# Kernel tuning notes

Hardware: AMD Instinct MI355X
Metric: run time of the kernel (lower is better)

The kernel has to match this reference:

```python
import jax, jax.numpy as jnp
import numpy as np

B, S, DM, DC, L, NS = 4, 2048, 2048, 512, 4, 5  # batch, seq, d_model, d_cortical, n_layers, n_settle


def _ln(x, g, b):
    # torch nn.LayerNorm, eps=1e-5
    m = x.mean(-1, keepdims=True)
    v = ((x - m) ** 2).mean(-1, keepdims=True)
    return (x - m) * jax.lax.rsqrt(v + 1e-5) * g + b


def setup_inputs() -> dict:
    key = jax.random.key(0)
    ks = jax.random.split(key, 20)
    f = lambda k, sh: jax.random.normal(k, sh, jnp.float32) * 0.02
    return dict(
        qwen_final_hidden=jax.random.normal(ks[0], (B, S, DM), jnp.float32),
        obs=jax.random.normal(ks[1], (4, B, S, DM), jnp.float32),
        proj_W=f(ks[2], (4, DC, DM)), proj_b=f(ks[3], (4, DC)),
        fuse_W=f(ks[4], (DC, 4 * DC)), fuse_b=f(ks[5], (DC,)),
        up_W=f(ks[6], (L, DC, DC)), up_b=f(ks[7], (L, DC)),
        lateral_W=f(ks[8], (L, DC, DC)), lateral_b=f(ks[9], (L, DC)),
        precision_logit=f(ks[10], (L, DC)),
        ln_g=jnp.ones((L, DC), jnp.float32), ln_b=jnp.zeros((L, DC), jnp.float32),
        down_W=f(ks[11], (L - 1, DC, DC)), down_b=f(ks[12], (L - 1, DC)),
        out1_W=f(ks[13], (DC, DC)), out1_b=f(ks[14], (DC,)),
        out2_W=f(ks[15], (DM, DC)), out2_b=f(ks[16], (DM,)),
    )


def reference(qwen_final_hidden, obs, proj_W, proj_b, fuse_W, fuse_b,
              up_W, up_b, lateral_W, lateral_b, precision_logit,
              ln_g, ln_b, down_W, down_b, out1_W, out1_b, out2_W, out2_b):
    b, s, dm = qwen_final_hidden.shape
    # per-observed-layer input projections, concatenated along features
    proj = jnp.einsum('obsd,ocd->bsoc', obs, proj_W) + proj_b  # (B,S,4,DC)
    cat = proj.reshape(b, s, -1)
    fused = cat @ fuse_W.T + fuse_b                             # (B,S,DC)
    x0 = fused.reshape(b * s, DC)                               # per-token cortical input

    prec = jax.nn.sigmoid(precision_logit)                      # (L,DC)

    # initial bottom-up pass: activations = compress(x)
    acts = []
    x = x0
    for i in range(L):
        x = _ln(x @ up_W[i].T + up_b[i], ln_g[i], ln_b[i])
        acts.append(x)

    # settling iterations
    for _ in range(NS):
        # top-down predictions computed from pre-sweep activations
        preds = [None] * L
        for i in range(L - 1, 0, -1):
            if i < L - 1:  # top layer has no top-down weights
                preds[i - 1] = acts[i] @ down_W[i].T + down_b[i]
        x = x0
        for i in range(L):
            compressed = _ln(x @ up_W[i].T + up_b[i], ln_g[i], ln_b[i])
            target = preds[i] if preds[i] is not None else acts[i]
            werr = (compressed - target) * prec[i]
            lateral = acts[i] @ lateral_W[i].T + lateral_b[i]
            acts[i] = _ln(acts[i] + 0.5 * werr + 0.1 * lateral, ln_g[i], ln_b[i])
            x = acts[i]

    top = acts[-1]
    h = jax.nn.gelu(top @ out1_W.T + out1_b, approximate=False)
    correction = (h @ out2_W.T + out2_b).reshape(b, s, dm)
    return qwen_final_hidden + correction
```

## Files before the change

kernel.cpp:

```cpp
#include <hip/hip_runtime.h>
#include <hip/hip_bf16.h>
#include <math.h>

#define NTOK 8192
#define DMD  2048
#define DCC  512
#define TOKH 4194304

typedef __attribute__((ext_vector_type(8))) short short8;
typedef __attribute__((ext_vector_type(4))) float f32x4;

__device__ inline float bf2f(unsigned short u) {
    union { unsigned int i; float f; } x; x.i = ((unsigned int)u) << 16; return x.f;
}
__device__ inline unsigned short f2bf(float f) {
    union { float f; unsigned int i; } x; x.f = f;
    unsigned int u = x.i;
    return (unsigned short)((u + 0x7fffu + ((u >> 16) & 1u)) >> 16);
}

typedef const __attribute__((address_space(1))) unsigned int* gas1_t;
typedef __attribute__((address_space(3))) unsigned int* las3_t;
__device__ inline void async16(const void* g, void* l) {
    __builtin_amdgcn_global_load_lds(
        (gas1_t)g,
        (las3_t)(unsigned int)(unsigned long long)l, 16, 0, 0);
}

__global__ __launch_bounds__(256)
void cvt_kernel(const float* __restrict__ s, unsigned short* __restrict__ d, int n4)
{
    int i = blockIdx.x * 256 + threadIdx.x;
    if (i >= n4) return;
    float4 v = ((const float4*)s)[i];
    ushort4 o;
    o.x = f2bf(v.x); o.y = f2bf(v.y); o.z = f2bf(v.z); o.w = f2bf(v.w);
    ((ushort4*)d)[i] = o;
}

struct CvtArgs { const float* src[7]; };

__global__ __launch_bounds__(256)
void wcvt_kernel(CvtArgs ca, unsigned short* __restrict__ dst)
{
    const int total = 2359296;
    for (int i = blockIdx.x * 256 + threadIdx.x; i < total; i += gridDim.x * 256) {
        const float* sp; int base;
        if      (i < 1048576) { sp = ca.src[0]; base = 0;       }
        else if (i < 1310720) { sp = ca.src[1]; base = 1048576; }
        else if (i < 1572864) { sp = ca.src[2]; base = 1310720; }
        else if (i < 1835008) { sp = ca.src[3]; base = 1572864; }
        else if (i < 2031616) { sp = ca.src[4]; base = 1835008; }
        else if (i < 2097152) { sp = ca.src[5]; base = 2031616; }
        else                  { sp = ca.src[6]; base = 2097152; }
        float4 v = ((const float4*)sp)[i - base];
        ushort4 o;
        o.x = f2bf(v.x); o.y = f2bf(v.y); o.z = f2bf(v.z); o.w = f2bf(v.w);
        ((ushort4*)dst)[i] = o;
    }
}

struct GArgs {
    const unsigned short* A[6];
    const unsigned short* W[6];
    const float*          bias[6];
    const float*          add[6];
    void*                 C[6];
};

template<bool OUTF32, bool GELU>
__global__ __launch_bounds__(256)
void gemm16(GArgs ga, int lda, int ldw, int ldadd, int ldc, int K)
{
    __shared__ unsigned short As[128 * 32];
    __shared__ unsigned short Bs[128 * 32];

    const int z    = blockIdx.z;
    const int tid  = threadIdx.x;
    const int wave = tid >> 6;
    const int lane = tid & 63;

    const int nwg   = gridDim.x * gridDim.y;
    const int bid   = blockIdx.y * gridDim.x + blockIdx.x;
    const int swz   = (bid & 7) * (nwg >> 3) + (bid >> 3);
    const int bn    = (swz % gridDim.x) * 128;
    const int bm    = (swz / gridDim.x) * 128;

    const int wr   = wave >> 1;
    const int wc   = wave & 1;

    const unsigned short* Ap = ga.A[z];
    const unsigned short* Wp = ga.W[z];

    const int lrow = lane >> 2;
    const int lcol = (lane & 3) * 8;

    f32x4 acc[4][4] = {};

    for (int k0 = 0; k0 < K; k0 += 32) {
        #pragma unroll
        for (int r = 0; r < 2; ++r) {
            int c = wave + r * 4;
            async16(Ap + (size_t)(bm + c * 16 + lrow) * lda + k0 + lcol, As + c * 512);
            async16(Wp + (size_t)(bn + c * 16 + lrow) * ldw + k0 + lcol, Bs + c * 512);
        }
        __syncthreads();

        short8 af[4], bfr[4];
        #pragma unroll
        for (int i = 0; i < 4; ++i) {
            af[i]  = *(const short8*)&As[(wr * 64 + i * 16 + (lane & 15)) * 32 + (lane >> 4) * 8];
            bfr[i] = *(const short8*)&Bs[(wc * 64 + i * 16 + (lane & 15)) * 32 + (lane >> 4) * 8];
        }
        #pragma unroll
        for (int mi = 0; mi < 4; ++mi)
            #pragma unroll
            for (int ni = 0; ni < 4; ++ni)
                acc[mi][ni] = __builtin_amdgcn_mfma_f32_16x16x32_bf16(
                    af[mi], bfr[ni], acc[mi][ni], 0, 0, 0);
        __syncthreads();
    }

    const float* bias = ga.bias[z];
    const float* add  = ga.add[z];
    #pragma unroll
    for (int ni = 0; ni < 4; ++ni) {
        int col = bn + wc * 64 + ni * 16 + (lane & 15);
        float bv = bias ? bias[col] : 0.0f;
        #pragma unroll
        for (int mi = 0; mi < 4; ++mi) {
            #pragma unroll
            for (int r = 0; r < 4; ++r) {
                int row = bm + wr * 64 + mi * 16 + (lane >> 4) * 4 + r;
                float vv = acc[mi][ni][r] + bv;
                if (GELU) vv = 0.5f * vv * (1.0f + erff(vv * 0.7071067811865475f));
                if (OUTF32) {
                    if (add) vv += add[(size_t)row * ldadd + col];
                    ((float*)ga.C[z])[(size_t)row * ldc + col] = vv;
                } else {
                    ((unsigned short*)ga.C[z])[(size_t)row * ldc + col] = f2bf(vv);
                }
            }
        }
    }
}

__device__ inline int csw(int rl, int col) {
    int s = ((rl >> 2) & 3) ^ (rl & 3);
    return rl * 512 + (col ^ (s << 4));
}

template<int MODE>
__global__ __launch_bounds__(512)
void gemm_fused(const unsigned short* __restrict__ Ap,
                const unsigned short* __restrict__ Wp,
                const float* __restrict__ bias,
                const float* __restrict__ g,
                const float* __restrict__ b,
                const unsigned short* a_in,
                const unsigned short* t_in,
                const unsigned short* __restrict__ lat_in,
                const float* __restrict__ logit,
                unsigned short* outp)
{
    __shared__ unsigned short Bs[2][512 * 32];
    __shared__ unsigned short As2[2][32 * 32];
    __shared__ float red[2][8][32];

    const int tid  = threadIdx.x;
    const int wave = tid >> 6;
    const int lane = tid & 63;
    const int lrow = lane >> 2;
    const int lc8  = (lane & 3) * 8;
    const int bm   = blockIdx.x * 32;
    const int l15  = lane & 15;
    const int lh   = lane >> 4;

    f32x4 acc[2][4] = {};

    if (wave < 2)
        async16(Ap + (size_t)(bm + wave * 16 + lrow) * DCC + lc8, &As2[0][wave * 512]);
    #pragma unroll
    for (int r = 0; r < 4; ++r)
        async16(Wp + (size_t)((r * 8 + wave) * 16 + lrow) * DCC + lc8,
                &Bs[0][(r * 8 + wave) * 512]);
    __syncthreads();

    for (int t = 0; t < 16; ++t) {
        const int cur = t & 1;
        if (t < 15) {
            const int k0 = (t + 1) * 32;
            if (wave < 2)
                async16(Ap + (size_t)(bm + wave * 16 + lrow) * DCC + k0 + lc8,
                        &As2[cur ^ 1][wave * 512]);
            #pragma unroll
            for (int r = 0; r < 4; ++r)
                async16(Wp + (size_t)((r * 8 + wave) * 16 + lrow) * DCC + k0 + lc8,
                        &Bs[cur ^ 1][(r * 8 + wave) * 512]);
        }
        short8 af[2], bfr[4];
        #pragma unroll
        for (int mi = 0; mi < 2; ++mi)
            af[mi] = *(const short8*)&As2[cur][(mi * 16 + l15) * 32 + lh * 8];
        #pragma unroll
        for (int ni = 0; ni < 4; ++ni)
            bfr[ni] = *(const short8*)&Bs[cur][(wave * 64 + ni * 16 + l15) * 32 + lh * 8];
        #pragma unroll
        for (int mi = 0; mi < 2; ++mi)
            #pragma unroll
            for (int ni = 0; ni < 4; ++ni)
                acc[mi][ni] = __builtin_amdgcn_mfma_f32_16x16x32_bf16(
                    af[mi], bfr[ni], acc[mi][ni], 0, 0, 0);
        __syncthreads();
    }

    float bv[4], gv[4], bbv[4];
    #pragma unroll
    for (int ni = 0; ni < 4; ++ni) {
        int col = wave * 64 + ni * 16 + l15;
        bv[ni] = bias[col]; gv[ni] = g[col]; bbv[ni] = b[col];
    }

    float ps[2][4], pq[2][4];
    #pragma unroll
    for (int mi = 0; mi < 2; ++mi)
        #pragma unroll
        for (int rr = 0; rr < 4; ++rr) {
            float s = 0.f, q = 0.f;
            #pragma unroll
            for (int ni = 0; ni < 4; ++ni) {
                float v = acc[mi][ni][rr] + bv[ni];
                acc[mi][ni][rr] = v;
                s += v; q += v * v;
            }
            #pragma unroll
            for (int off = 1; off < 16; off <<= 1) {
                s += __shfl_xor(s, off, 64);
                q += __shfl_xor(q, off, 64);
            }
            ps[mi][rr] = s; pq[mi][rr] = q;
        }
    if (l15 == 0) {
        #pragma unroll
        for (int mi = 0; mi < 2; ++mi)
            #pragma unroll
            for (int rr = 0; rr < 4; ++rr) {
                int rl = mi * 16 + lh * 4 + rr;
                red[0][wave][rl] = ps[mi][rr];
                red[1][wave][rl] = pq[mi][rr];
            }
    }
    __syncthreads();

    unsigned short* compS = &Bs[0][0];
    #pragma unroll
    for (int mi = 0; mi < 2; ++mi)
        #pragma unroll
        for (int rr = 0; rr < 4; ++rr) {
            int rl = mi * 16 + lh * 4 + rr;
            float s = 0.f, q = 0.f;
            #pragma unroll
            for (int w = 0; w < 8; ++w) { s += red[0][w][rl]; q += red[1][w][rl]; }
            float m1 = s * (1.0f / DCC);
            float r1 = rsqrtf(q * (1.0f / DCC) - m1 * m1 + 1e-5f);
            #pragma unroll
            for (int ni = 0; ni < 4; ++ni) {
                int col = wave * 64 + ni * 16 + l15;
                compS[csw(rl, col)] = f2bf((acc[mi][ni][rr] - m1) * r1 * gv[ni] + bbv[ni]);
            }
        }
    __syncthreads();

    const int c0 = lane * 8;
    if constexpr (MODE == 0) {
        #pragma unroll
        for (int rr = 0; rr < 4; ++rr) {
            const int rl = wave * 4 + rr;
            const size_t gbase = (size_t)(bm + rl) * DCC + c0;
            short8 cm = *(const short8*)&compS[csw(rl, c0)];
            *(short8*)(outp + gbase) = cm;
        }
    } else {
        float gr[8], br[8], pr[8];
        {
            float4 g0 = *(const float4*)(g + c0),     g1 = *(const float4*)(g + c0 + 4);
            float4 b0 = *(const float4*)(b + c0),     b1 = *(const float4*)(b + c0 + 4);
            float4 p0 = *(const float4*)(logit + c0), p1 = *(const float4*)(logit + c0 + 4);
            float gt[8] = {g0.x,g0.y,g0.z,g0.w,g1.x,g1.y,g1.z,g1.w};
            float bt[8] = {b0.x,b0.y,b0.z,b0.w,b1.x,b1.y,b1.z,b1.w};
            float pt[8] = {p0.x,p0.y,p0.z,p0.w,p1.x,p1.y,p1.z,p1.w};
            #pragma unroll
            for (int j = 0; j < 8; ++j) {
                gr[j] = gt[j]; br[j] = bt[j];
                pr[j] = 1.0f / (1.0f + __expf(-pt[j]));
            }
        }
        #pragma unroll
        for (int rr = 0; rr < 4; ++rr) {
            const int rl = wave * 4 + rr;
            const size_t gbase = (size_t)(bm + rl) * DCC + c0;
            short8 cm = *(const short8*)&compS[csw(rl, c0)];
            short8 ar = *(const short8*)(a_in + gbase);
            short8 tr = *(const short8*)(t_in + gbase);
            short8 lr = *(const short8*)(lat_in + gbase);
            float tv[8], s = 0.f, q = 0.f;
            #pragma unroll
            for (int j = 0; j < 8; ++j) {
                float val = bf2f((unsigned short)ar[j])
                          + 0.5f * (bf2f((unsigned short)cm[j]) - bf2f((unsigned short)tr[j])) * pr[j]
                          + 0.1f * bf2f((unsigned short)lr[j]);
                tv[j] = val; s += val; q += val * val;
            }
            #pragma unroll
            for (int off = 1; off < 64; off <<= 1) {
                s += __shfl_xor(s, off, 64);
                q += __shfl_xor(q, off, 64);
            }
            float m2 = s * (1.0f / DCC);
            float r2 = rsqrtf(q * (1.0f / DCC) - m2 * m2 + 1e-5f);
            short8 o;
            #pragma unroll
            for (int j = 0; j < 8; ++j)
                o[j] = (short)f2bf((tv[j] - m2) * r2 * gr[j] + br[j]);
            *(short8*)(outp + gbase) = o;
        }
    }
}

extern "C" void kernel_launch(void* const* d_in, const int* in_sizes, int n_in,
                              void* d_out, int out_size, void* d_ws, size_t ws_size,
                              hipStream_t stream)
{
    const float* qwen   = (const float*)d_in[0];
    const float* obs    = (const float*)d_in[1];
    const float* proj_W = (const float*)d_in[2];
    const float* proj_b = (const float*)d_in[3];
    const float* fuse_W = (const float*)d_in[4];
    const float* fuse_b = (const float*)d_in[5];
    const float* up_W   = (const float*)d_in[6];
    const float* up_b   = (const float*)d_in[7];
    const float* lat_W  = (const float*)d_in[8];
    const float* lat_b  = (const float*)d_in[9];
    const float* plogit = (const float*)d_in[10];
    const float* ln_g   = (const float*)d_in[11];
    const float* ln_b   = (const float*)d_in[12];
    const float* down_W = (const float*)d_in[13];
    const float* down_b = (const float*)d_in[14];
    const float* out1_W = (const float*)d_in[15];
    const float* out1_b = (const float*)d_in[16];
    const float* out2_W = (const float*)d_in[17];
    const float* out2_b = (const float*)d_in[18];
    float* out = (float*)d_out;

    unsigned short* wsu = (unsigned short*)d_ws;
    unsigned short* catbuf = wsu;
    unsigned short* x0b    = wsu + 16777216;
    unsigned short* acts16[4] = {
        wsu + 20971520, wsu + 20971520 + TOKH,
        wsu + 20971520 + 2 * TOKH, wsu + 20971520 + 3 * TOKH };
    unsigned short* w16    = wsu + 37748736;
    unsigned short* projW16 = w16;
    unsigned short* fuseW16 = w16 + 4194304;
    unsigned short* upW16   = w16 + 5242880;
    unsigned short* latW16  = w16 + 6291456;
    unsigned short* downW16 = w16 + 7340032;
    unsigned short* out1W16 = w16 + 8126464;
    unsigned short* out2W16 = w16 + 8388608;
    unsigned short* obs16   = wsu + 47185920;
    unsigned short* h16     = catbuf;

    unsigned short* outu = (unsigned short*)d_out;
    unsigned short* pred16a = outu;
    unsigned short* pred16b = outu + TOKH;
    unsigned short* lat16[4] = { outu + 2*TOKH, outu + 3*TOKH, outu + 4*TOKH, outu + 5*TOKH };

    dim3 blk(256);
    dim3 blk512(512);

    {
        CvtArgs ca;
        ca.src[0] = proj_W; ca.src[1] = fuse_W; ca.src[2] = up_W;
        ca.src[3] = lat_W;  ca.src[4] = down_W; ca.src[5] = out1_W;
        ca.src[6] = out2_W;
        wcvt_kernel<<<dim3(2048), blk, 0, stream>>>(ca, w16);
    }

    {
        int n4 = (4 * NTOK * DMD) / 4;
        cvt_kernel<<<dim3(n4 / 256), blk, 0, stream>>>(obs, obs16, n4);
        GArgs a{};
        for (int o = 0; o < 4; ++o) {
            a.A[o]    = obs16 + (size_t)o * NTOK * DMD;
            a.W[o]    = projW16 + (size_t)o * DCC * DMD;
            a.bias[o] = proj_b + o * DCC;
            a.C[o]    = catbuf + o * DCC;
        }
        gemm16<false, false><<<dim3(DCC/128, NTOK/128, 4), blk, 0, stream>>>(
            a, DMD, DMD, 0, 4 * DCC, DMD);
    }
    {
        GArgs a{};
        a.A[0] = catbuf; a.W[0] = fuseW16; a.bias[0] = fuse_b; a.C[0] = x0b;
        gemm16<false, false><<<dim3(DCC/128, NTOK/128, 1), blk, 0, stream>>>(
            a, 4 * DCC, 4 * DCC, 0, DCC, 4 * DCC);
    }

    dim3 fgrid(NTOK / 32);

    for (int i = 0; i < 4; ++i) {
        gemm_fused<0><<<fgrid, blk512, 0, stream>>>(
            (i == 0) ? x0b : acts16[i - 1],
            upW16 + (size_t)i * DCC * DCC, up_b + i * DCC,
            ln_g + i * DCC, ln_b + i * DCC,
            nullptr, nullptr, nullptr, nullptr, acts16[i]);
    }

    for (int s = 0; s < 5; ++s) {
        {
            GArgs a{};
            a.A[0] = acts16[1]; a.W[0] = downW16 + (size_t)1 * DCC * DCC;
            a.bias[0] = down_b + 1 * DCC; a.C[0] = pred16a;
            a.A[1] = acts16[2]; a.W[1] = downW16 + (size_t)2 * DCC * DCC;
            a.bias[1] = down_b + 2 * DCC; a.C[1] = pred16b;
            for (int i = 0; i < 4; ++i) {
                a.A[2 + i] = acts16[i];
                a.W[2 + i] = latW16 + (size_t)i * DCC * DCC;
                a.bias[2 + i] = lat_b + i * DCC;
                a.C[2 + i] = lat16[i];
            }
            gemm16<false, false><<<dim3(DCC/128, NTOK/128, 6), blk, 0, stream>>>(
                a, DCC, DCC, 0, DCC, DCC);
        }
        for (int i = 0; i < 4; ++i) {
            const unsigned short* tgt =
                (i == 0) ? pred16a : (i == 1) ? pred16b : acts16[i];
            gemm_fused<1><<<fgrid, blk512, 0, stream>>>(
                (i == 0) ? x0b : acts16[i - 1],
                upW16 + (size_t)i * DCC * DCC, up_b + i * DCC,
                ln_g + i * DCC, ln_b + i * DCC,
                acts16[i], tgt, lat16[i], plogit + i * DCC, acts16[i]);
        }
    }

    {
        GArgs a{};
        a.A[0] = acts16[3]; a.W[0] = out1W16; a.bias[0] = out1_b; a.C[0] = h16;
        gemm16<false, true><<<dim3(DCC/128, NTOK/128, 1), blk, 0, stream>>>(
            a, DCC, DCC, 0, DCC, DCC);
    }
    {
        GArgs a{};
        a.A[0] = h16; a.W[0] = out2W16; a.bias[0] = out2_b;
        a.add[0] = qwen; a.C[0] = out;
        gemm16<true, false><<<dim3(DMD/128, NTOK/128, 1), blk, 0, stream>>>(
            a, DCC, DCC, DMD, DMD, DCC);
    }
}
```

Baseline: 1.574 ms.

## Fold fuse weights into projection weights and read fp32 obs directly

Precomputes the product of the fuse matrix and each projection matrix (plus a folded bias), so x0 is computed by one GEMM from obs straight to DC outputs instead of projecting to a 4*DC concat buffer and then fusing. The new x0gemm kernel converts fp32 obs to bf16 while loading each tile, which removes the separate obs conversion pass and its large bf16 buffer write and read. This removes the intermediate catbuf traffic and the second GEMM. In exchange it adds a small weight-product GEMM, a transpose kernel and a bias kernel, and rounds the combined matrix to bf16, which changes numerics slightly.

```diff
diff --git a/kernel.cpp b/kernel.cpp
--- a/kernel.cpp
+++ b/kernel.cpp
@@ -27,37 +27,68 @@
         (las3_t)(unsigned int)(unsigned long long)l, 16, 0, 0);
 }
 
-__global__ __launch_bounds__(256)
-void cvt_kernel(const float* __restrict__ s, unsigned short* __restrict__ d, int n4)
-{
-    int i = blockIdx.x * 256 + threadIdx.x;
-    if (i >= n4) return;
-    float4 v = ((const float4*)s)[i];
-    ushort4 o;
-    o.x = f2bf(v.x); o.y = f2bf(v.y); o.z = f2bf(v.z); o.w = f2bf(v.w);
-    ((ushort4*)d)[i] = o;
-}
-
-struct CvtArgs { const float* src[7]; };
+struct CvtArgs { const float* src[6]; };
 
 __global__ __launch_bounds__(256)
 void wcvt_kernel(CvtArgs ca, unsigned short* __restrict__ dst)
 {
-    const int total = 2359296;
+    const int total = 1310720;
     for (int i = blockIdx.x * 256 + threadIdx.x; i < total; i += gridDim.x * 256) {
         const float* sp; int base;
-        if      (i < 1048576) { sp = ca.src[0]; base = 0;       }
-        else if (i < 1310720) { sp = ca.src[1]; base = 1048576; }
-        else if (i < 1572864) { sp = ca.src[2]; base = 1310720; }
-        else if (i < 1835008) { sp = ca.src[3]; base = 1572864; }
-        else if (i < 2031616) { sp = ca.src[4]; base = 1835008; }
-        else if (i < 2097152) { sp = ca.src[5]; base = 2031616; }
-        else                  { sp = ca.src[6]; base = 2097152; }
+        if      (i <  262144) { sp = ca.src[0]; base = 0;       }
+        else if (i <  524288) { sp = ca.src[1]; base = 262144;  }
+        else if (i <  786432) { sp = ca.src[2]; base = 524288;  }
+        else if (i <  983040) { sp = ca.src[3]; base = 786432;  }
+        else if (i < 1048576) { sp = ca.src[4]; base = 983040;  }
+        else                  { sp = ca.src[5]; base = 1048576; }
         float4 v = ((const float4*)sp)[i - base];
         ushort4 o;
         o.x = f2bf(v.x); o.y = f2bf(v.y); o.z = f2bf(v.z); o.w = f2bf(v.w);
         ((ushort4*)dst)[i] = o;
     }
+}
+
+__global__ __launch_bounds__(256)
+void ptr_kernel(const float* __restrict__ src, unsigned short* __restrict__ dst)
+{
+    __shared__ float t[32][33];
+    const int o  = blockIdx.z;
+    const int jb = blockIdx.x * 32;
+    const int kb = blockIdx.y * 32;
+    const int r  = threadIdx.x >> 3;
+    const int c4 = (threadIdx.x & 7) * 4;
+    {
+        const float* s = src + ((size_t)o * DCC + kb + r) * DMD + jb + c4;
+        float4 v = *(const float4*)s;
+        t[r][c4+0]=v.x; t[r][c4+1]=v.y; t[r][c4+2]=v.z; t[r][c4+3]=v.w;
+    }
+    __syncthreads();
+    {
+        ushort4 u;
+        u.x = f2bf(t[c4+0][r]); u.y = f2bf(t[c4+1][r]);
+        u.z = f2bf(t[c4+2][r]); u.w = f2bf(t[c4+3][r]);
+        *(ushort4*)(dst + ((size_t)o * DMD + jb + r) * DCC + kb + c4) = u;
+    }
+}
+
+__global__ __launch_bounds__(256)
+void bprime_kernel(const float* __restrict__ fuse_W, const float* __restrict__ fuse_b,
+                   const float* __restrict__ proj_b, float* __restrict__ bp)
+{
+    const int row = blockIdx.x * 8 + (threadIdx.x >> 5);
+    const int l32 = threadIdx.x & 31;
+    const float* r = fuse_W + (size_t)row * (4 * DCC) + l32 * 64;
+    const float* p = proj_b + l32 * 64;
+    float s = 0.f;
+    #pragma unroll
+    for (int k = 0; k < 64; k += 4) {
+        float4 v = *(const float4*)(r + k);
+        float4 q = *(const float4*)(p + k);
+        s += v.x*q.x + v.y*q.y + v.z*q.z + v.w*q.w;
+    }
+    #pragma unroll
+    for (int off = 16; off; off >>= 1) s += __shfl_xor(s, off, 64);
+    if (l32 == 0) bp[row] = s + fuse_b[row];
 }
 
 struct GArgs {
@@ -142,6 +173,89 @@
                 }
             }
         }
+    }
+}
+
+__global__ __launch_bounds__(256)
+void x0gemm(const float* __restrict__ obs,
+            const unsigned short* __restrict__ M16,
+            const float* __restrict__ bp,
+            unsigned short* __restrict__ x0)
+{
+    __shared__ unsigned short As[64 * 32];
+    __shared__ unsigned short Bs[128 * 32];
+
+    const int tid  = threadIdx.x;
+    const int wave = tid >> 6;
+    const int lane = tid & 63;
+
+    const int nwg = gridDim.x * gridDim.y;
+    const int bid = blockIdx.y * gridDim.x + blockIdx.x;
+    const int swz = (bid & 7) * (nwg >> 3) + (bid >> 3);
+    const int bn  = (swz % gridDim.x) * 128;
+    const int bm  = (swz / gridDim.x) * 64;
+
+    const int wr = wave >> 1;
+    const int wc = wave & 1;
+    const int lrow = lane >> 2;
+    const int lcol = (lane & 3) * 8;
+    const int arow = tid >> 2;
+    const int ac8  = (tid & 3) * 8;
+    const int l15  = lane & 15;
+    const int lh   = lane >> 4;
+
+    f32x4 acc[2][4] = {};
+
+    for (int o = 0; o < 4; ++o) {
+        const float* Ap = obs + (size_t)o * NTOK * DMD;
+        const unsigned short* Wp = M16 + (size_t)o * DCC * DMD;
+        for (int k0 = 0; k0 < DMD; k0 += 32) {
+            #pragma unroll
+            for (int r = 0; r < 2; ++r) {
+                int c = wave + r * 4;
+                async16(Wp + (size_t)(bn + c * 16 + lrow) * DMD + k0 + lcol, Bs + c * 512);
+            }
+            {
+                const float* s = Ap + (size_t)(bm + arow) * DMD + k0 + ac8;
+                float4 v0 = *(const float4*)(s);
+                float4 v1 = *(const float4*)(s + 4);
+                short8 o8;
+                o8[0]=(short)f2bf(v0.x); o8[1]=(short)f2bf(v0.y);
+                o8[2]=(short)f2bf(v0.z); o8[3]=(short)f2bf(v0.w);
+                o8[4]=(short)f2bf(v1.x); o8[5]=(short)f2bf(v1.y);
+                o8[6]=(short)f2bf(v1.z); o8[7]=(short)f2bf(v1.w);
+                *(short8*)&As[arow * 32 + ac8] = o8;
+            }
+            __syncthreads();
+
+            short8 af[2], bfr[4];
+            #pragma unroll
+            for (int i = 0; i < 2; ++i)
+                af[i] = *(const short8*)&As[(wr * 32 + i * 16 + l15) * 32 + lh * 8];
+            #pragma unroll
+            for (int i = 0; i < 4; ++i)
+                bfr[i] = *(const short8*)&Bs[(wc * 64 + i * 16 + l15) * 32 + lh * 8];
+            #pragma unroll
+            for (int mi = 0; mi < 2; ++mi)
+                #pragma unroll
+                for (int ni = 0; ni < 4; ++ni)
+                    acc[mi][ni] = __builtin_amdgcn_mfma_f32_16x16x32_bf16(
+                        af[mi], bfr[ni], acc[mi][ni], 0, 0, 0);
+            __syncthreads();
+        }
+    }
+
+    #pragma unroll
+    for (int ni = 0; ni < 4; ++ni) {
+        int col = bn + wc * 64 + ni * 16 + l15;
+        float bv = bp[col];
+        #pragma unroll
+        for (int mi = 0; mi < 2; ++mi)
+            #pragma unroll
+            for (int r = 0; r < 4; ++r) {
+                int row = bm + wr * 32 + mi * 16 + lh * 4 + r;
+                x0[(size_t)row * DCC + col] = f2bf(acc[mi][ni][r] + bv);
+            }
     }
 }
 
@@ -353,21 +467,21 @@
     float* out = (float*)d_out;
 
     unsigned short* wsu = (unsigned short*)d_ws;
-    unsigned short* catbuf = wsu;
+    float*          bp     = (float*)wsu;
+    unsigned short* h16    = wsu + 2048;
     unsigned short* x0b    = wsu + 16777216;
     unsigned short* acts16[4] = {
         wsu + 20971520, wsu + 20971520 + TOKH,
         wsu + 20971520 + 2 * TOKH, wsu + 20971520 + 3 * TOKH };
     unsigned short* w16    = wsu + 37748736;
-    unsigned short* projW16 = w16;
-    unsigned short* fuseW16 = w16 + 4194304;
-    unsigned short* upW16   = w16 + 5242880;
-    unsigned short* latW16  = w16 + 6291456;
-    unsigned short* downW16 = w16 + 7340032;
-    unsigned short* out1W16 = w16 + 8126464;
-    unsigned short* out2W16 = w16 + 8388608;
-    unsigned short* obs16   = wsu + 47185920;
-    unsigned short* h16     = catbuf;
+    unsigned short* fuseW16 = w16;
+    unsigned short* upW16   = w16 + 1048576;
+    unsigned short* latW16  = w16 + 2097152;
+    unsigned short* downW16 = w16 + 3145728;
+    unsigned short* out1W16 = w16 + 3932160;
+    unsigned short* out2W16 = w16 + 4194304;
+    unsigned short* projT16 = wsu + 47185920;
+    unsigned short* M16     = wsu + 51380224;
 
     unsigned short* outu = (unsigned short*)d_out;
     unsigned short* pred16a = outu;
@@ -379,31 +493,26 @@
 
     {
         CvtArgs ca;
-        ca.src[0] = proj_W; ca.src[1] = fuse_W; ca.src[2] = up_W;
-        ca.src[3] = lat_W;  ca.src[4] = down_W; ca.src[5] = out1_W;
-        ca.src[6] = out2_W;
+        ca.src[0] = fuse_W; ca.src[1] = up_W;   ca.src[2] = lat_W;
+        ca.src[3] = down_W; ca.src[4] = out1_W; ca.src[5] = out2_W;
         wcvt_kernel<<<dim3(2048), blk, 0, stream>>>(ca, w16);
     }
+    ptr_kernel<<<dim3(DMD/32, DCC/32, 4), blk, 0, stream>>>(proj_W, projT16);
+    bprime_kernel<<<dim3(DCC/8), blk, 0, stream>>>(fuse_W, fuse_b, proj_b, bp);
 
     {
-        int n4 = (4 * NTOK * DMD) / 4;
-        cvt_kernel<<<dim3(n4 / 256), blk, 0, stream>>>(obs, obs16, n4);
         GArgs a{};
         for (int o = 0; o < 4; ++o) {
-            a.A[o]    = obs16 + (size_t)o * NTOK * DMD;
-            a.W[o]    = projW16 + (size_t)o * DCC * DMD;
-            a.bias[o] = proj_b + o * DCC;
-            a.C[o]    = catbuf + o * DCC;
-        }
-        gemm16<false, false><<<dim3(DCC/128, NTOK/128, 4), blk, 0, stream>>>(
-            a, DMD, DMD, 0, 4 * DCC, DMD);
-    }
-    {
-        GArgs a{};
-        a.A[0] = catbuf; a.W[0] = fuseW16; a.bias[0] = fuse_b; a.C[0] = x0b;
-        gemm16<false, false><<<dim3(DCC/128, NTOK/128, 1), blk, 0, stream>>>(
-            a, 4 * DCC, 4 * DCC, 0, DCC, 4 * DCC);
-    }
+            a.A[o] = fuseW16 + o * DCC;
+            a.W[o] = projT16 + (size_t)o * DMD * DCC;
+            a.bias[o] = nullptr;
+            a.C[o] = M16 + (size_t)o * DCC * DMD;
+        }
+        gemm16<false, false><<<dim3(DMD/128, DCC/128, 4), blk, 0, stream>>>(
+            a, 4 * DCC, DCC, 0, DMD, DCC);
+    }
+
+    x0gemm<<<dim3(DCC/128, NTOK/64), blk, 0, stream>>>(obs, M16, bp, x0b);
 
     dim3 fgrid(NTOK / 32);
 
```

Result: no change. 1.583 ms (+0.5%).
